# Kernel optimization log

Hardware: AMD Instinct MI355X
Metric: run time of the kernel (lower is better)

## Reference

```python
import jax, jax.numpy as jnp
import numpy as np

B, T, IN, Z, S = 256, 1024, 64, 512, 2
H = Z - S  # 510
MHU = 1.5


def setup_inputs() -> dict:
    key = jax.random.key(0)
    ks = jax.random.split(key, 12)
    sc = 0.05
    return {
        "rnn_input": jax.random.normal(ks[0], (B, T, IN), jnp.float32),
        "tau": jax.random.uniform(ks[1], (B, T, 1), jnp.float32),
        "z0": jax.random.normal(ks[2], (1, B, Z), jnp.float32),
        "cz0": jax.random.normal(ks[3], (1, B, Z), jnp.float32),
        # LSTMCell: W: (IN+S) -> 4H with bias, U: H -> 4H no bias
        "W_w": jax.random.normal(ks[4], (4 * H, IN + S), jnp.float32) * sc,
        "W_b": jax.random.normal(ks[5], (4 * H,), jnp.float32) * sc,
        "U_w": jax.random.normal(ks[6], (4 * H, H), jnp.float32) * sc,
        "alpha_w": jax.random.normal(ks[7], (S, H), jnp.float32) * sc,
        "alpha_b": jax.random.normal(ks[8], (S,), jnp.float32) * sc,
        "hx_w": jax.random.normal(ks[9], (S, H), jnp.float32) * sc,
        "hx_b": jax.random.normal(ks[10], (S,), jnp.float32) * sc,
    }


def reference(rnn_input, tau, z0, cz0, W_w, W_b, U_w, alpha_w, alpha_b, hx_w, hx_b):
    dt = rnn_input.dtype
    # fixed continuous-time system matrix (state_dim = 2)
    A = jnp.array([[MHU, -MHU], [1.0 / MHU, 0.0]], dtype=dt)

    x0 = z0[0, :, :S]       # [B, S]
    h0 = z0[0, :, S:]       # [B, H]
    c0 = cz0[0, :, S:]      # [B, H]
    cx = cz0[0, :, :S]      # [B, S], carried unchanged

    def step(carry, xs):
        x_prev, h, c = carry
        inp_t, tau_t = xs                                   # [B,IN], [B,1]
        u = jnp.concatenate([x_prev, inp_t], axis=1)        # [B, S+IN]
        gates = u @ W_w.T + W_b + h @ U_w.T                 # [B, 4H]
        i, f, g, o = jnp.split(gates, 4, axis=1)
        i = jax.nn.sigmoid(i)
        f = jax.nn.sigmoid(f)
        g = jnp.tanh(g)
        o = jax.nn.sigmoid(o)
        c_new = f * c + i * g
        h_new = o * jnp.tanh(c_new)
        # forward-Euler discretisation: x_mid = (I + tau*A) x_prev
        x_mid = x_prev + tau_t * (x_prev @ A.T)             # [B, S]
        alpha = jax.nn.sigmoid(h_new @ alpha_w.T + alpha_b) # [B, S]
        x_next = (1.0 - alpha) * x_mid + alpha * (h_new @ hx_w.T + hx_b)
        out = jnp.concatenate([x_next, h_new], axis=1)      # [B, Z]
        return (x_next, h_new, c_new), out

    xs = (jnp.swapaxes(rnn_input, 0, 1), jnp.swapaxes(tau, 0, 1))  # time-major
    (xT, hT, cT), outs = jax.lax.scan(step, (x0, h0, c0), xs)
    outputs = jnp.swapaxes(outs, 0, 1)                      # [B, T, Z]
    z_fin = jnp.concatenate([xT, hT], axis=1)[None]         # [1, B, Z]
    cz_fin = jnp.concatenate([cx, cT], axis=1)[None]        # [1, B, Z]
    return outputs, (z_fin, cz_fin)
```

## Files before the change

kernel.cpp:

```cpp
#include <hip/hip_runtime.h>

typedef unsigned short u16;
typedef unsigned int u32;
typedef unsigned long long u64;
typedef __attribute__((ext_vector_type(8))) short s16x8;
typedef __attribute__((ext_vector_type(4))) short s16x4;
typedef __attribute__((ext_vector_type(4))) float f32x4;

#define TSTEPS 1024
#define PSTR   584
#define ZOFF   ((size_t)134217728)
#define CZOFF  (ZOFF + 131072)

#define CNT_OFF 0
#define HB_OFF  1024
#define WK_OFF  525312
#define WX_OFF  2884608
#define WB_OFF  2900992
#define AW_OFF  2909184
#define AB_OFF  2913280

__device__ __forceinline__ float bf2f(u16 h) { union { unsigned u; float f; } c; c.u = ((unsigned)h) << 16; return c.f; }
__device__ __forceinline__ u16 f2bf(float f) { union { float f; unsigned u; } c; c.f = f; unsigned u = c.u; return (u16)((u + 0x7FFFu + ((u >> 16) & 1u)) >> 16); }
__device__ __forceinline__ float fsigm(float x) { return __builtin_amdgcn_rcpf(1.f + __builtin_amdgcn_exp2f(-1.44269504089f * x)); }
__device__ __forceinline__ float ftanh(float x) { float t = __builtin_amdgcn_exp2f(2.88539008178f * x); return 1.f - 2.f * __builtin_amdgcn_rcpf(t + 1.f); }
__device__ __forceinline__ float pick4(float a, float b, float c, float d, int m) {
  return (m == 0) ? a : (m == 1) ? b : (m == 2) ? c : d;
}
#define NTS(p, v) __builtin_nontemporal_store((v), (p))

#if defined(__has_builtin)
#if __has_builtin(__builtin_amdgcn_fdot2_f32_bf16)
#define HAVE_DOT2 1
typedef __bf16 bf16x2 __attribute__((ext_vector_type(2)));
#endif
#endif

__device__ __forceinline__ float dot2acc(u32 h2, u32 a2, float acc) {
#ifdef HAVE_DOT2
  bf16x2 hv, av;
  __builtin_memcpy(&hv, &h2, 4);
  __builtin_memcpy(&av, &a2, 4);
  return __builtin_amdgcn_fdot2_f32_bf16(hv, av, acc, false);
#else
  acc += bf2f((u16)(h2 & 0xFFFFu)) * bf2f((u16)(a2 & 0xFFFFu));
  acc += bf2f((u16)(h2 >> 16)) * bf2f((u16)(a2 >> 16));
  return acc;
#endif
}

__global__ void prep_pack(const float* __restrict__ W_w, const float* __restrict__ W_b,
                          const float* __restrict__ U_w, const float* __restrict__ alpha_w,
                          const float* __restrict__ alpha_b, const float* __restrict__ hx_w,
                          const float* __restrict__ hx_b,
                          u16* __restrict__ wk, float* __restrict__ wx, float* __restrict__ wb,
                          u16* __restrict__ aw, float* __restrict__ ab, unsigned* __restrict__ cnt)
{
  int n = blockIdx.x;
  int tid = threadIdx.x;
  if (n < 2048) {
    int j = n >> 2, g = n & 3;
    bool real = (j < 510);
    int row = g * 510 + j;
    for (int k = tid; k < 576; k += 64) {
      float v = 0.f;
      if (real) {
        if (k < 64) v = W_w[row * 66 + 2 + k];
        else { int kk = k - 64; v = (kk < 510) ? U_w[row * 510 + kk] : 0.f; }
      }
      wk[(size_t)n * 576 + k] = f2bf(v);
    }
    if (tid == 0) {
      wx[n * 2 + 0] = real ? W_w[row * 66 + 0] : 0.f;
      wx[n * 2 + 1] = real ? W_w[row * 66 + 1] : 0.f;
      wb[n] = real ? W_b[row] : 0.f;
    }
    if (n == 0 && tid < 16)
      __hip_atomic_store(&cnt[tid * 16], 0u, __ATOMIC_RELAXED, __HIP_MEMORY_SCOPE_AGENT);
  } else {
    int s = n - 2048;
    for (int j = tid; j < 512; j += 64) {
      float v = 0.f;
      if (j < 510) v = (s < 2) ? alpha_w[s * 510 + j] : hx_w[(s - 2) * 510 + j];
      aw[s * 512 + j] = f2bf(v);
    }
    if (tid == 0) ab[s] = (s < 2) ? alpha_b[s] : hx_b[s - 2];
  }
}

__global__ void prep_h0(const float* __restrict__ z0, u16* __restrict__ hb0)
{
  int b = blockIdx.x;
  int j = threadIdx.x * 4;
#pragma unroll
  for (int e = 0; e < 4; ++e) {
    int jj = j + e;
    hb0[(size_t)b * 512 + jj] = (jj < 510) ? f2bf(z0[(size_t)b * 512 + 2 + jj]) : (u16)0;
  }
}

extern "C" __global__ void __launch_bounds__(256, 1)
lstm_persist(const float* __restrict__ rnn, const float* __restrict__ tau,
             const float* __restrict__ z0, const float* __restrict__ cz0,
             const u16* __restrict__ wk, const float* __restrict__ wx, const float* __restrict__ wb,
             const u16* __restrict__ aw, const float* __restrict__ ab,
             u16* __restrict__ hbuf, unsigned* __restrict__ cnt,
             float* __restrict__ out)
{
  __shared__ u16   u_sh[16 * PSTR];
  __shared__ float xs_sh[16 * 2];

  const int tid = threadIdx.x;
  const int bid = blockIdx.x;
  const int grp = bid & 15;
  const int w   = bid >> 4;
  const int bb0 = grp * 16;
  const int v   = tid >> 6;
  const int l   = tid & 63;
  const int l15 = l & 15, l4 = l >> 4;
  const int n0  = w * 128 + v * 32;
  const int prow = tid >> 4;
  const int jc   = tid & 15;

  u32 awr[4][4][4];
  {
    const u32* awp = (const u32*)aw;
#pragma unroll
    for (int s = 0; s < 4; ++s)
#pragma unroll
      for (int q = 0; q < 4; ++q)
#pragma unroll
        for (int p = 0; p < 4; ++p)
          awr[s][q][p] = awp[(s * 512 + jc * 32 + q * 8) / 2 + p];
  }
  float ab0 = ab[0], ab1 = ab[1], ab2 = ab[2], ab3 = ab[3];

  s16x8 bfr[36];
  {
    const u16* wb0 = wk + (size_t)(n0 + l15) * 576 + l4 * 8;
#pragma unroll
    for (int kf = 0; kf < 18; ++kf) {
      bfr[2 * kf + 0] = *(const s16x8*)(wb0 + kf * 32);
      bfr[2 * kf + 1] = *(const s16x8*)(wb0 + 16 * 576 + kf * 32);
    }
  }
  float wxf[2][2], wbf[2];
  {
    int nA = n0 + l15, nB = nA + 16;
    wxf[0][0] = wx[nA * 2]; wxf[0][1] = wx[nA * 2 + 1];
    wxf[1][0] = wx[nB * 2]; wxf[1][1] = wx[nB * 2 + 1];
    wbf[0] = wb[nA]; wbf[1] = wb[nB];
  }
  float cst[2][4];
#pragma unroll
  for (int nf = 0; nf < 2; ++nf) {
    int j = (n0 + nf * 16 + l15) >> 2;
#pragma unroll
    for (int r = 0; r < 4; ++r) {
      int b = bb0 + 4 * l4 + r;
      cst[nf][r] = (j < 510) ? cz0[(size_t)b * 512 + 2 + j] : 0.f;
    }
  }
  {
    const float* ip = rnn + (size_t)(bb0 + prow) * (TSTEPS * 64) + jc * 4;
    float4 inpv = *(const float4*)ip;
    s16x4 iv;
    iv[0] = (short)f2bf(inpv.x); iv[1] = (short)f2bf(inpv.y);
    iv[2] = (short)f2bf(inpv.z); iv[3] = (short)f2bf(inpv.w);
    *(s16x4*)(&u_sh[prow * PSTR + jc * 4]) = iv;
  }
  __syncthreads();

  const int g = l & 3;
  const float sc_a = (g == 2) ? -2.88539008178f : -1.44269504089f;
  const float sc_m = (g == 2) ? 2.f : 1.f;
  const float sc_c = (g == 2) ? -1.f : 0.f;

  unsigned* mycnt = cnt + grp * 16;
  float tv_reg = 0.f;

  for (int t = 0; t <= TSTEPS; ++t) {
    u16* hb = hbuf + (size_t)(t & 1) * (256 * 512) + (size_t)bb0 * 512;
    u64 q0, q1, q2, q3, q4, q5, q6, q7;
    {
      u64* hp = (u64*)hb + (size_t)tid * 8;
      q0 = __hip_atomic_load(hp + 0, __ATOMIC_RELAXED, __HIP_MEMORY_SCOPE_AGENT);
      q1 = __hip_atomic_load(hp + 1, __ATOMIC_RELAXED, __HIP_MEMORY_SCOPE_AGENT);
      q2 = __hip_atomic_load(hp + 2, __ATOMIC_RELAXED, __HIP_MEMORY_SCOPE_AGENT);
      q3 = __hip_atomic_load(hp + 3, __ATOMIC_RELAXED, __HIP_MEMORY_SCOPE_AGENT);
      q4 = __hip_atomic_load(hp + 4, __ATOMIC_RELAXED, __HIP_MEMORY_SCOPE_AGENT);
      q5 = __hip_atomic_load(hp + 5, __ATOMIC_RELAXED, __HIP_MEMORY_SCOPE_AGENT);
      q6 = __hip_atomic_load(hp + 6, __ATOMIC_RELAXED, __HIP_MEMORY_SCOPE_AGENT);
      q7 = __hip_atomic_load(hp + 7, __ATOMIC_RELAXED, __HIP_MEMORY_SCOPE_AGENT);
    }
    u32 h32[16];
    h32[0] = (u32)q0; h32[1] = (u32)(q0 >> 32); h32[2]  = (u32)q1; h32[3]  = (u32)(q1 >> 32);
    h32[4] = (u32)q2; h32[5] = (u32)(q2 >> 32); h32[6]  = (u32)q3; h32[7]  = (u32)(q3 >> 32);
    h32[8] = (u32)q4; h32[9] = (u32)(q4 >> 32); h32[10] = (u32)q5; h32[11] = (u32)(q5 >> 32);
    h32[12] = (u32)q6; h32[13] = (u32)(q6 >> 32); h32[14] = (u32)q7; h32[15] = (u32)(q7 >> 32);

    float s0 = 0.f, s1 = 0.f, s2 = 0.f, s3 = 0.f;
#pragma unroll
    for (int q = 0; q < 4; ++q) {
#pragma unroll
      for (int p = 0; p < 4; ++p) {
        u32 h2 = h32[4 * q + p];
        s0 = dot2acc(h2, awr[0][q][p], s0);
        s1 = dot2acc(h2, awr[1][q][p], s1);
        s2 = dot2acc(h2, awr[2][q][p], s2);
        s3 = dot2acc(h2, awr[3][q][p], s3);
      }
    }
#pragma unroll
    for (int m = 1; m <= 8; m <<= 1) {
      s0 += __shfl_xor(s0, m, 64);
      s1 += __shfl_xor(s1, m, 64);
      s2 += __shfl_xor(s2, m, 64);
      s3 += __shfl_xor(s3, m, 64);
    }
    {
      u16* ur = &u_sh[prow * PSTR + 64 + jc * 32];
      u64 t2[2];
      t2[0] = q0; t2[1] = q1; __builtin_memcpy(ur + 0, t2, 16);
      t2[0] = q2; t2[1] = q3; __builtin_memcpy(ur + 8, t2, 16);
      t2[0] = q4; t2[1] = q5; __builtin_memcpy(ur + 16, t2, 16);
      t2[0] = q6; t2[1] = q7; __builtin_memcpy(ur + 24, t2, 16);
    }
    if ((l & 15) == 0) {
      int row = prow;
      float xn0, xn1;
      if (t == 0) {
        xn0 = z0[(size_t)(bb0 + row) * 512 + 0];
        xn1 = z0[(size_t)(bb0 + row) * 512 + 1];
      } else {
        float x0p = xs_sh[row * 2 + 0], x1p = xs_sh[row * 2 + 1];
        float tv = tv_reg;
        float a0v = fsigm(s0 + ab0);
        float a1v = fsigm(s1 + ab1);
        float hx0 = s2 + ab2, hx1 = s3 + ab3;
        float xm0 = x0p + tv * (1.5f * x0p - 1.5f * x1p);
        float xm1 = x1p + tv * (0.6666666667f * x0p);
        xn0 = (1.f - a0v) * xm0 + a0v * hx0;
        xn1 = (1.f - a1v) * xm1 + a1v * hx1;
      }
      xs_sh[row * 2 + 0] = xn0; xs_sh[row * 2 + 1] = xn1;
    }
    __syncthreads();

    if (t == TSTEPS) {
      int j2 = tid * 2;
      if (j2 < 510) {
        unsigned hv2 = *(const unsigned*)&u_sh[w * PSTR + 64 + j2];
        float h0 = bf2f((u16)(hv2 & 0xFFFFu));
        float h1 = bf2f((u16)(hv2 >> 16));
        size_t ob = ((size_t)(bb0 + w) * TSTEPS + (TSTEPS - 1)) * 512 + 2 + j2;
        NTS(&out[ob], h0); NTS(&out[ob + 1], h1);
        size_t zb = ZOFF + (size_t)(bb0 + w) * 512 + 2 + j2;
        NTS(&out[zb], h0); NTS(&out[zb + 1], h1);
      }
      if ((l & 15) == 0 && w == prow) {
        int b = bb0 + prow;
        float xn0 = xs_sh[prow * 2 + 0], xn1 = xs_sh[prow * 2 + 1];
        float* ob = out + ((size_t)b * TSTEPS + (TSTEPS - 1)) * 512;
        NTS(ob + 0, xn0); NTS(ob + 1, xn1);
        NTS(&out[ZOFF + (size_t)b * 512 + 0], xn0);
        NTS(&out[ZOFF + (size_t)b * 512 + 1], xn1);
        NTS(&out[CZOFF + (size_t)b * 512 + 0], cz0[(size_t)b * 512 + 0]);
        NTS(&out[CZOFF + (size_t)b * 512 + 1], cz0[(size_t)b * 512 + 1]);
      }
      break;
    }

    f32x4 acc0 = {0.f, 0.f, 0.f, 0.f};
    f32x4 acc1 = {0.f, 0.f, 0.f, 0.f};
    {
      const u16* ap = &u_sh[l15 * PSTR + l4 * 8];
#pragma unroll
      for (int kf = 0; kf < 18; ++kf) {
        s16x8 a = *(const s16x8*)(ap + kf * 32);
        acc0 = __builtin_amdgcn_mfma_f32_16x16x32_bf16(a, bfr[2 * kf + 0], acc0, 0, 0, 0);
        acc1 = __builtin_amdgcn_mfma_f32_16x16x32_bf16(a, bfr[2 * kf + 1], acc1, 0, 0, 0);
      }
    }
    u16* hout = hbuf + (size_t)((t + 1) & 1) * (256 * 512);
    float xr[4][2];
#pragma unroll
    for (int r = 0; r < 4; ++r) {
      xr[r][0] = xs_sh[(4 * l4 + r) * 2 + 0];
      xr[r][1] = xs_sh[(4 * l4 + r) * 2 + 1];
    }
    float myh0 = 0.f, myh1 = 0.f;
#pragma unroll
    for (int nf = 0; nf < 2; ++nf) {
      f32x4 av = nf ? acc1 : acc0;
#pragma unroll
      for (int r = 0; r < 4; ++r) {
        float pre = av[r] + wbf[nf] + xr[r][0] * wxf[nf][0] + xr[r][1] * wxf[nf][1];
        float y = __builtin_amdgcn_rcpf(1.f + __builtin_amdgcn_exp2f(sc_a * pre));
        float act = y * sc_m + sc_c;
        float vB = __shfl_xor(act, 1, 64);
        float vC = __shfl_xor(act, 2, 64);
        float vD = __shfl_xor(vB, 2, 64);
        float si = pick4(act, vB, vC, vD, g);
        float sf = pick4(act, vB, vC, vD, g ^ 1);
        float tg = pick4(act, vB, vC, vD, g ^ 2);
        float so = pick4(act, vB, vC, vD, g ^ 3);
        float cn = sf * cst[nf][r] + si * tg;
        cst[nf][r] = cn;
        float hn = so * ftanh(cn);
        if (g == r) { if (nf == 0) myh0 = hn; else myh1 = hn; }
      }
    }
    {
      int row = 4 * l4 + g;
      u32 mine = (u32)f2bf(myh0) | ((u32)f2bf(myh1) << 16);
      u32 oth = (u32)__shfl_xor((int)mine, 4, 64);
      if (((l15 >> 2) & 1) == 0) {
        int j0 = (n0 >> 2) + (l15 >> 2);
        u32 v0 = (mine & 0xFFFFu) | ((oth & 0xFFFFu) << 16);
        u32 v1 = (mine >> 16) | (oth & 0xFFFF0000u);
        u32* hp = (u32*)(hout + (size_t)(bb0 + row) * 512);
        __hip_atomic_store(hp + (j0 >> 1), v0, __ATOMIC_RELAXED, __HIP_MEMORY_SCOPE_AGENT);
        __hip_atomic_store(hp + (j0 >> 1) + 2, v1, __ATOMIC_RELAXED, __HIP_MEMORY_SCOPE_AGENT);
      }
    }
    __syncthreads();
    if (tid == 0) {
      asm volatile("s_waitcnt vmcnt(0)" ::: "memory");
      __hip_atomic_fetch_add(mycnt, 1u, __ATOMIC_RELAXED, __HIP_MEMORY_SCOPE_AGENT);
    }
    if (t >= 1) {
      int j2 = tid * 2;
      if (j2 < 510) {
        unsigned hv2 = *(const unsigned*)&u_sh[w * PSTR + 64 + j2];
        float h0 = bf2f((u16)(hv2 & 0xFFFFu));
        float h1 = bf2f((u16)(hv2 >> 16));
        size_t ob = ((size_t)(bb0 + w) * TSTEPS + (t - 1)) * 512 + 2 + j2;
        NTS(&out[ob], h0); NTS(&out[ob + 1], h1);
      }
      if ((l & 15) == 0 && w == prow) {
        float* ob = out + ((size_t)(bb0 + prow) * TSTEPS + (t - 1)) * 512;
        NTS(ob + 0, xs_sh[prow * 2 + 0]); NTS(ob + 1, xs_sh[prow * 2 + 1]);
      }
    }
    if (t + 1 < TSTEPS) {
      const float* ip = rnn + (size_t)(bb0 + prow) * (TSTEPS * 64) + (size_t)(t + 1) * 64 + jc * 4;
      float4 inpv = *(const float4*)ip;
      s16x4 iv;
      iv[0] = (short)f2bf(inpv.x); iv[1] = (short)f2bf(inpv.y);
      iv[2] = (short)f2bf(inpv.z); iv[3] = (short)f2bf(inpv.w);
      *(s16x4*)(&u_sh[prow * PSTR + jc * 4]) = iv;
    }
    if ((l & 15) == 0) {
      tv_reg = tau[(size_t)(bb0 + prow) * TSTEPS + t];
    }
    if (tid == 0) {
      unsigned tgt = 16u * (unsigned)(t + 1);
      while (__hip_atomic_load(mycnt, __ATOMIC_RELAXED, __HIP_MEMORY_SCOPE_AGENT) < tgt) {
        __builtin_amdgcn_s_sleep(1);
      }
    }
    __syncthreads();
  }

#pragma unroll
  for (int nf = 0; nf < 2; ++nf) {
    int j = (n0 + nf * 16 + l15) >> 2;
    if (j < 510) {
#pragma unroll
      for (int r = 0; r < 4; ++r) {
        if ((l & 3) == r) {
          NTS(&out[CZOFF + (size_t)(bb0 + 4 * l4 + r) * 512 + 2 + j], cst[nf][r]);
        }
      }
    }
  }
}

extern "C" void kernel_launch(void* const* d_in, const int* in_sizes, int n_in,
                              void* d_out, int out_size, void* d_ws, size_t ws_size,
                              hipStream_t stream) {
  const float* rnn     = (const float*)d_in[0];
  const float* tau     = (const float*)d_in[1];
  const float* z0      = (const float*)d_in[2];
  const float* cz0     = (const float*)d_in[3];
  const float* W_w     = (const float*)d_in[4];
  const float* W_b     = (const float*)d_in[5];
  const float* U_w     = (const float*)d_in[6];
  const float* alpha_w = (const float*)d_in[7];
  const float* alpha_b = (const float*)d_in[8];
  const float* hx_w    = (const float*)d_in[9];
  const float* hx_b    = (const float*)d_in[10];

  char* ws = (char*)d_ws;
  unsigned* cnt = (unsigned*)(ws + CNT_OFF);
  u16*      hb  = (u16*)(ws + HB_OFF);
  u16*      wk  = (u16*)(ws + WK_OFF);
  float*    wx  = (float*)(ws + WX_OFF);
  float*    wbv = (float*)(ws + WB_OFF);
  u16*      awv = (u16*)(ws + AW_OFF);
  float*    abv = (float*)(ws + AB_OFF);

  hipLaunchKernelGGL(prep_pack, dim3(2052), dim3(64), 0, stream,
                     W_w, W_b, U_w, alpha_w, alpha_b, hx_w, hx_b, wk, wx, wbv, awv, abv, cnt);
  hipLaunchKernelGGL(prep_h0, dim3(256), dim3(128), 0, stream, z0, hb);
  hipLaunchKernelGGL(lstm_persist, dim3(256), dim3(256), 0, stream,
                     rnn, tau, z0, cz0, wk, wx, wbv, awv, abv, hb, cnt, (float*)d_out);
}
```

Baseline: 5.441 ms.

## Replace block-wide barrier spin with per-wave counters and double-buffered shared state

```diff
diff --git a/kernel.cpp b/kernel.cpp
--- a/kernel.cpp
+++ b/kernel.cpp
@@ -13,12 +13,12 @@
 #define CZOFF  (ZOFF + 131072)
 
 #define CNT_OFF 0
-#define HB_OFF  1024
-#define WK_OFF  525312
-#define WX_OFF  2884608
-#define WB_OFF  2900992
-#define AW_OFF  2909184
-#define AB_OFF  2913280
+#define HB_OFF  4096
+#define WK_OFF  (HB_OFF + 524288)
+#define WX_OFF  (WK_OFF + 2359296)
+#define WB_OFF  (WX_OFF + 16384)
+#define AW_OFF  (WB_OFF + 8192)
+#define AB_OFF  (AW_OFF + 4096)
 
 __device__ __forceinline__ float bf2f(u16 h) { union { unsigned u; float f; } c; c.u = ((unsigned)h) << 16; return c.f; }
 __device__ __forceinline__ u16 f2bf(float f) { union { float f; unsigned u; } c; c.f = f; unsigned u = c.u; return (u16)((u + 0x7FFFu + ((u >> 16) & 1u)) >> 16); }
@@ -28,6 +28,7 @@
   return (m == 0) ? a : (m == 1) ? b : (m == 2) ? c : d;
 }
 #define NTS(p, v) __builtin_nontemporal_store((v), (p))
+#define AL(p) __hip_atomic_load((p), __ATOMIC_RELAXED, __HIP_MEMORY_SCOPE_AGENT)
 
 #if defined(__has_builtin)
 #if __has_builtin(__builtin_amdgcn_fdot2_f32_bf16)
@@ -75,7 +76,7 @@
       wx[n * 2 + 1] = real ? W_w[row * 66 + 1] : 0.f;
       wb[n] = real ? W_b[row] : 0.f;
     }
-    if (n == 0 && tid < 16)
+    if (n == 0)
       __hip_atomic_store(&cnt[tid * 16], 0u, __ATOMIC_RELAXED, __HIP_MEMORY_SCOPE_AGENT);
   } else {
     int s = n - 2048;
@@ -107,8 +108,8 @@
              u16* __restrict__ hbuf, unsigned* __restrict__ cnt,
              float* __restrict__ out)
 {
-  __shared__ u16   u_sh[16 * PSTR];
-  __shared__ float xs_sh[16 * 2];
+  __shared__ u16   u_sh[2][16 * PSTR];
+  __shared__ float xs_sh[2][16 * 2];
 
   const int tid = threadIdx.x;
   const int bid = blockIdx.x;
@@ -167,7 +168,7 @@
     s16x4 iv;
     iv[0] = (short)f2bf(inpv.x); iv[1] = (short)f2bf(inpv.y);
     iv[2] = (short)f2bf(inpv.z); iv[3] = (short)f2bf(inpv.w);
-    *(s16x4*)(&u_sh[prow * PSTR + jc * 4]) = iv;
+    *(s16x4*)(&u_sh[0][prow * PSTR + jc * 4]) = iv;
   }
   __syncthreads();
 
@@ -176,22 +177,29 @@
   const float sc_m = (g == 2) ? 2.f : 1.f;
   const float sc_c = (g == 2) ? -1.f : 0.f;
 
-  unsigned* mycnt = cnt + grp * 16;
+  unsigned* cvec = cnt + grp * 64;
+  unsigned* myslot = cvec + v * 16;
   float tv_reg = 0.f;
 
   for (int t = 0; t <= TSTEPS; ++t) {
-    u16* hb = hbuf + (size_t)(t & 1) * (256 * 512) + (size_t)bb0 * 512;
+    const int cur = t & 1;
+    if (t > 0) {
+      unsigned tgt = 16u * (unsigned)t;
+      for (;;) {
+        u32 c0 = AL(cvec + 0);
+        u32 c1 = AL(cvec + 16);
+        u32 c2 = AL(cvec + 32);
+        u32 c3 = AL(cvec + 48);
+        if ((c0 >= tgt) & (c1 >= tgt) & (c2 >= tgt) & (c3 >= tgt)) break;
+      }
+      asm volatile("" ::: "memory");
+    }
+    u16* hb = hbuf + (size_t)cur * (256 * 512) + (size_t)bb0 * 512;
     u64 q0, q1, q2, q3, q4, q5, q6, q7;
     {
       u64* hp = (u64*)hb + (size_t)tid * 8;
-      q0 = __hip_atomic_load(hp + 0, __ATOMIC_RELAXED, __HIP_MEMORY_SCOPE_AGENT);
-      q1 = __hip_atomic_load(hp + 1, __ATOMIC_RELAXED, __HIP_MEMORY_SCOPE_AGENT);
-      q2 = __hip_atomic_load(hp + 2, __ATOMIC_RELAXED, __HIP_MEMORY_SCOPE_AGENT);
-      q3 = __hip_atomic_load(hp + 3, __ATOMIC_RELAXED, __HIP_MEMORY_SCOPE_AGENT);
-      q4 = __hip_atomic_load(hp + 4, __ATOMIC_RELAXED, __HIP_MEMORY_SCOPE_AGENT);
-      q5 = __hip_atomic_load(hp + 5, __ATOMIC_RELAXED, __HIP_MEMORY_SCOPE_AGENT);
-      q6 = __hip_atomic_load(hp + 6, __ATOMIC_RELAXED, __HIP_MEMORY_SCOPE_AGENT);
-      q7 = __hip_atomic_load(hp + 7, __ATOMIC_RELAXED, __HIP_MEMORY_SCOPE_AGENT);
+      q0 = AL(hp + 0); q1 = AL(hp + 1); q2 = AL(hp + 2); q3 = AL(hp + 3);
+      q4 = AL(hp + 4); q5 = AL(hp + 5); q6 = AL(hp + 6); q7 = AL(hp + 7);
     }
     u32 h32[16];
     h32[0] = (u32)q0; h32[1] = (u32)(q0 >> 32); h32[2]  = (u32)q1; h32[3]  = (u32)(q1 >> 32);
@@ -219,7 +227,7 @@
       s3 += __shfl_xor(s3, m, 64);
     }
     {
-      u16* ur = &u_sh[prow * PSTR + 64 + jc * 32];
+      u16* ur = &u_sh[cur][prow * PSTR + 64 + jc * 32];
       u64 t2[2];
       t2[0] = q0; t2[1] = q1; __builtin_memcpy(ur + 0, t2, 16);
       t2[0] = q2; t2[1] = q3; __builtin_memcpy(ur + 8, t2, 16);
@@ -233,7 +241,7 @@
         xn0 = z0[(size_t)(bb0 + row) * 512 + 0];
         xn1 = z0[(size_t)(bb0 + row) * 512 + 1];
       } else {
-        float x0p = xs_sh[row * 2 + 0], x1p = xs_sh[row * 2 + 1];
+        float x0p = xs_sh[cur ^ 1][row * 2 + 0], x1p = xs_sh[cur ^ 1][row * 2 + 1];
         float tv = tv_reg;
         float a0v = fsigm(s0 + ab0);
         float a1v = fsigm(s1 + ab1);
@@ -243,14 +251,14 @@
         xn0 = (1.f - a0v) * xm0 + a0v * hx0;
         xn1 = (1.f - a1v) * xm1 + a1v * hx1;
       }
-      xs_sh[row * 2 + 0] = xn0; xs_sh[row * 2 + 1] = xn1;
+      xs_sh[cur][row * 2 + 0] = xn0; xs_sh[cur][row * 2 + 1] = xn1;
     }
     __syncthreads();
 
     if (t == TSTEPS) {
       int j2 = tid * 2;
       if (j2 < 510) {
-        unsigned hv2 = *(const unsigned*)&u_sh[w * PSTR + 64 + j2];
+        unsigned hv2 = *(const unsigned*)&u_sh[cur][w * PSTR + 64 + j2];
         float h0 = bf2f((u16)(hv2 & 0xFFFFu));
         float h1 = bf2f((u16)(hv2 >> 16));
         size_t ob = ((size_t)(bb0 + w) * TSTEPS + (TSTEPS - 1)) * 512 + 2 + j2;
@@ -260,7 +268,7 @@
       }
       if ((l & 15) == 0 && w == prow) {
         int b = bb0 + prow;
-        float xn0 = xs_sh[prow * 2 + 0], xn1 = xs_sh[prow * 2 + 1];
+        float xn0 = xs_sh[cur][prow * 2 + 0], xn1 = xs_sh[cur][prow * 2 + 1];
         float* ob = out + ((size_t)b * TSTEPS + (TSTEPS - 1)) * 512;
         NTS(ob + 0, xn0); NTS(ob + 1, xn1);
         NTS(&out[ZOFF + (size_t)b * 512 + 0], xn0);
@@ -274,7 +282,7 @@
     f32x4 acc0 = {0.f, 0.f, 0.f, 0.f};
     f32x4 acc1 = {0.f, 0.f, 0.f, 0.f};
     {
-      const u16* ap = &u_sh[l15 * PSTR + l4 * 8];
+      const u16* ap = &u_sh[cur][l15 * PSTR + l4 * 8];
 #pragma unroll
       for (int kf = 0; kf < 18; ++kf) {
         s16x8 a = *(const s16x8*)(ap + kf * 32);
@@ -282,12 +290,12 @@
         acc1 = __builtin_amdgcn_mfma_f32_16x16x32_bf16(a, bfr[2 * kf + 1], acc1, 0, 0, 0);
       }
     }
-    u16* hout = hbuf + (size_t)((t + 1) & 1) * (256 * 512);
+    u16* hout = hbuf + (size_t)(cur ^ 1) * (256 * 512);
     float xr[4][2];
 #pragma unroll
     for (int r = 0; r < 4; ++r) {
-      xr[r][0] = xs_sh[(4 * l4 + r) * 2 + 0];
-      xr[r][1] = xs_sh[(4 * l4 + r) * 2 + 1];
+      xr[r][0] = xs_sh[cur][(4 * l4 + r) * 2 + 0];
+      xr[r][1] = xs_sh[cur][(4 * l4 + r) * 2 + 1];
     }
     float myh0 = 0.f, myh1 = 0.f;
 #pragma unroll
@@ -324,15 +332,13 @@
         __hip_atomic_store(hp + (j0 >> 1) + 2, v1, __ATOMIC_RELAXED, __HIP_MEMORY_SCOPE_AGENT);
       }
     }
-    __syncthreads();
-    if (tid == 0) {
-      asm volatile("s_waitcnt vmcnt(0)" ::: "memory");
-      __hip_atomic_fetch_add(mycnt, 1u, __ATOMIC_RELAXED, __HIP_MEMORY_SCOPE_AGENT);
-    }
+    asm volatile("s_waitcnt vmcnt(0)" ::: "memory");
+    if (l == 0)
+      __hip_atomic_fetch_add(myslot, 1u, __ATOMIC_RELAXED, __HIP_MEMORY_SCOPE_AGENT);
     if (t >= 1) {
       int j2 = tid * 2;
       if (j2 < 510) {
-        unsigned hv2 = *(const unsigned*)&u_sh[w * PSTR + 64 + j2];
+        unsigned hv2 = *(const unsigned*)&u_sh[cur][w * PSTR + 64 + j2];
         float h0 = bf2f((u16)(hv2 & 0xFFFFu));
         float h1 = bf2f((u16)(hv2 >> 16));
         size_t ob = ((size_t)(bb0 + w) * TSTEPS + (t - 1)) * 512 + 2 + j2;
@@ -340,7 +346,7 @@
       }
       if ((l & 15) == 0 && w == prow) {
         float* ob = out + ((size_t)(bb0 + prow) * TSTEPS + (t - 1)) * 512;
-        NTS(ob + 0, xs_sh[prow * 2 + 0]); NTS(ob + 1, xs_sh[prow * 2 + 1]);
+        NTS(ob + 0, xs_sh[cur][prow * 2 + 0]); NTS(ob + 1, xs_sh[cur][prow * 2 + 1]);
       }
     }
     if (t + 1 < TSTEPS) {
@@ -349,18 +355,11 @@
       s16x4 iv;
       iv[0] = (short)f2bf(inpv.x); iv[1] = (short)f2bf(inpv.y);
       iv[2] = (short)f2bf(inpv.z); iv[3] = (short)f2bf(inpv.w);
-      *(s16x4*)(&u_sh[prow * PSTR + jc * 4]) = iv;
+      *(s16x4*)(&u_sh[cur ^ 1][prow * PSTR + jc * 4]) = iv;
     }
     if ((l & 15) == 0) {
       tv_reg = tau[(size_t)(bb0 + prow) * TSTEPS + t];
     }
-    if (tid == 0) {
-      unsigned tgt = 16u * (unsigned)(t + 1);
-      while (__hip_atomic_load(mycnt, __ATOMIC_RELAXED, __HIP_MEMORY_SCOPE_AGENT) < tgt) {
-        __builtin_amdgcn_s_sleep(1);
-      }
-    }
-    __syncthreads();
   }
 
 #pragma unroll
```

After: 5.492 ms. Within noise of the previous version (+0.9%).

## Replace atomic counter barrier with per-block step flags polled at step start

Applied to the files above, without the earlier changes.

```diff
diff --git a/kernel.cpp b/kernel.cpp
--- a/kernel.cpp
+++ b/kernel.cpp
@@ -6,13 +6,14 @@
 typedef __attribute__((ext_vector_type(8))) short s16x8;
 typedef __attribute__((ext_vector_type(4))) short s16x4;
 typedef __attribute__((ext_vector_type(4))) float f32x4;
+typedef __attribute__((ext_vector_type(2))) float f32x2;
 
 #define TSTEPS 1024
 #define PSTR   584
 #define ZOFF   ((size_t)134217728)
 #define CZOFF  (ZOFF + 131072)
 
-#define CNT_OFF 0
+#define ST_OFF  0
 #define HB_OFF  1024
 #define WK_OFF  525312
 #define WX_OFF  2884608
@@ -54,7 +55,7 @@
                           const float* __restrict__ alpha_b, const float* __restrict__ hx_w,
                           const float* __restrict__ hx_b,
                           u16* __restrict__ wk, float* __restrict__ wx, float* __restrict__ wb,
-                          u16* __restrict__ aw, float* __restrict__ ab, unsigned* __restrict__ cnt)
+                          u16* __restrict__ aw, float* __restrict__ ab, u32* __restrict__ stmp)
 {
   int n = blockIdx.x;
   int tid = threadIdx.x;
@@ -75,8 +76,11 @@
       wx[n * 2 + 1] = real ? W_w[row * 66 + 1] : 0.f;
       wb[n] = real ? W_b[row] : 0.f;
     }
-    if (n == 0 && tid < 16)
-      __hip_atomic_store(&cnt[tid * 16], 0u, __ATOMIC_RELAXED, __HIP_MEMORY_SCOPE_AGENT);
+    if (n == 0) {
+#pragma unroll
+      for (int k = 0; k < 4; ++k)
+        __hip_atomic_store(&stmp[tid * 4 + k], 0u, __ATOMIC_RELAXED, __HIP_MEMORY_SCOPE_AGENT);
+    }
   } else {
     int s = n - 2048;
     for (int j = tid; j < 512; j += 64) {
@@ -104,11 +108,11 @@
              const float* __restrict__ z0, const float* __restrict__ cz0,
              const u16* __restrict__ wk, const float* __restrict__ wx, const float* __restrict__ wb,
              const u16* __restrict__ aw, const float* __restrict__ ab,
-             u16* __restrict__ hbuf, unsigned* __restrict__ cnt,
+             u16* __restrict__ hbuf, u32* __restrict__ stmp,
              float* __restrict__ out)
 {
   __shared__ u16   u_sh[16 * PSTR];
-  __shared__ float xs_sh[16 * 2];
+  __shared__ float xs_sh[2][32];
 
   const int tid = threadIdx.x;
   const int bid = blockIdx.x;
@@ -176,11 +180,20 @@
   const float sc_m = (g == 2) ? 2.f : 1.f;
   const float sc_c = (g == 2) ? -1.f : 0.f;
 
-  unsigned* mycnt = cnt + grp * 16;
+  u32* sl = stmp + grp * 16;
   float tv_reg = 0.f;
 
   for (int t = 0; t <= TSTEPS; ++t) {
-    u16* hb = hbuf + (size_t)(t & 1) * (256 * 512) + (size_t)bb0 * 512;
+    const int cur = t & 1;
+    if (t > 0) {
+      const u32 tgt = (u32)t;
+      for (;;) {
+        u32 sv = __hip_atomic_load(&sl[jc], __ATOMIC_RELAXED, __HIP_MEMORY_SCOPE_AGENT);
+        if (__ballot(sv >= tgt) == ~0ull) break;
+      }
+      asm volatile("" ::: "memory");
+    }
+    u16* hb = hbuf + (size_t)cur * (256 * 512) + (size_t)bb0 * 512;
     u64 q0, q1, q2, q3, q4, q5, q6, q7;
     {
       u64* hp = (u64*)hb + (size_t)tid * 8;
@@ -199,6 +212,21 @@
     h32[8] = (u32)q4; h32[9] = (u32)(q4 >> 32); h32[10] = (u32)q5; h32[11] = (u32)(q5 >> 32);
     h32[12] = (u32)q6; h32[13] = (u32)(q6 >> 32); h32[14] = (u32)q7; h32[15] = (u32)(q7 >> 32);
 
+    if (t >= 1 && prow == w) {
+      float* ob = out + ((size_t)(bb0 + w) * TSTEPS + (t - 1)) * 512 + 2 + jc * 32;
+#pragma unroll
+      for (int p = 0; p < 16; ++p) {
+        int col = jc * 32 + 2 * p;
+        if (col < 510) {
+          u32 h2 = h32[p];
+          f32x2 fv;
+          fv[0] = bf2f((u16)(h2 & 0xFFFFu));
+          fv[1] = bf2f((u16)(h2 >> 16));
+          NTS((f32x2*)(ob + 2 * p), fv);
+        }
+      }
+    }
+
     float s0 = 0.f, s1 = 0.f, s2 = 0.f, s3 = 0.f;
 #pragma unroll
     for (int q = 0; q < 4; ++q) {
@@ -233,7 +261,7 @@
         xn0 = z0[(size_t)(bb0 + row) * 512 + 0];
         xn1 = z0[(size_t)(bb0 + row) * 512 + 1];
       } else {
-        float x0p = xs_sh[row * 2 + 0], x1p = xs_sh[row * 2 + 1];
+        float x0p = xs_sh[cur ^ 1][row * 2 + 0], x1p = xs_sh[cur ^ 1][row * 2 + 1];
         float tv = tv_reg;
         float a0v = fsigm(s0 + ab0);
         float a1v = fsigm(s1 + ab1);
@@ -243,7 +271,7 @@
         xn0 = (1.f - a0v) * xm0 + a0v * hx0;
         xn1 = (1.f - a1v) * xm1 + a1v * hx1;
       }
-      xs_sh[row * 2 + 0] = xn0; xs_sh[row * 2 + 1] = xn1;
+      xs_sh[cur][row * 2 + 0] = xn0; xs_sh[cur][row * 2 + 1] = xn1;
     }
     __syncthreads();
 
@@ -253,14 +281,12 @@
         unsigned hv2 = *(const unsigned*)&u_sh[w * PSTR + 64 + j2];
         float h0 = bf2f((u16)(hv2 & 0xFFFFu));
         float h1 = bf2f((u16)(hv2 >> 16));
-        size_t ob = ((size_t)(bb0 + w) * TSTEPS + (TSTEPS - 1)) * 512 + 2 + j2;
-        NTS(&out[ob], h0); NTS(&out[ob + 1], h1);
         size_t zb = ZOFF + (size_t)(bb0 + w) * 512 + 2 + j2;
         NTS(&out[zb], h0); NTS(&out[zb + 1], h1);
       }
       if ((l & 15) == 0 && w == prow) {
         int b = bb0 + prow;
-        float xn0 = xs_sh[prow * 2 + 0], xn1 = xs_sh[prow * 2 + 1];
+        float xn0 = xs_sh[cur][prow * 2 + 0], xn1 = xs_sh[cur][prow * 2 + 1];
         float* ob = out + ((size_t)b * TSTEPS + (TSTEPS - 1)) * 512;
         NTS(ob + 0, xn0); NTS(ob + 1, xn1);
         NTS(&out[ZOFF + (size_t)b * 512 + 0], xn0);
@@ -282,12 +308,12 @@
         acc1 = __builtin_amdgcn_mfma_f32_16x16x32_bf16(a, bfr[2 * kf + 1], acc1, 0, 0, 0);
       }
     }
-    u16* hout = hbuf + (size_t)((t + 1) & 1) * (256 * 512);
+    u16* hout = hbuf + (size_t)(cur ^ 1) * (256 * 512);
     float xr[4][2];
 #pragma unroll
     for (int r = 0; r < 4; ++r) {
-      xr[r][0] = xs_sh[(4 * l4 + r) * 2 + 0];
-      xr[r][1] = xs_sh[(4 * l4 + r) * 2 + 1];
+      xr[r][0] = xs_sh[cur][(4 * l4 + r) * 2 + 0];
+      xr[r][1] = xs_sh[cur][(4 * l4 + r) * 2 + 1];
     }
     float myh0 = 0.f, myh1 = 0.f;
 #pragma unroll
@@ -327,21 +353,11 @@
     __syncthreads();
     if (tid == 0) {
       asm volatile("s_waitcnt vmcnt(0)" ::: "memory");
-      __hip_atomic_fetch_add(mycnt, 1u, __ATOMIC_RELAXED, __HIP_MEMORY_SCOPE_AGENT);
-    }
-    if (t >= 1) {
-      int j2 = tid * 2;
-      if (j2 < 510) {
-        unsigned hv2 = *(const unsigned*)&u_sh[w * PSTR + 64 + j2];
-        float h0 = bf2f((u16)(hv2 & 0xFFFFu));
-        float h1 = bf2f((u16)(hv2 >> 16));
-        size_t ob = ((size_t)(bb0 + w) * TSTEPS + (t - 1)) * 512 + 2 + j2;
-        NTS(&out[ob], h0); NTS(&out[ob + 1], h1);
-      }
-      if ((l & 15) == 0 && w == prow) {
-        float* ob = out + ((size_t)(bb0 + prow) * TSTEPS + (t - 1)) * 512;
-        NTS(ob + 0, xs_sh[prow * 2 + 0]); NTS(ob + 1, xs_sh[prow * 2 + 1]);
-      }
+      __hip_atomic_store(&sl[w], (u32)(t + 1), __ATOMIC_RELAXED, __HIP_MEMORY_SCOPE_AGENT);
+    }
+    if (t >= 1 && (l & 15) == 0 && w == prow) {
+      float* ob = out + ((size_t)(bb0 + prow) * TSTEPS + (t - 1)) * 512;
+      NTS(ob + 0, xs_sh[cur][prow * 2 + 0]); NTS(ob + 1, xs_sh[cur][prow * 2 + 1]);
     }
     if (t + 1 < TSTEPS) {
       const float* ip = rnn + (size_t)(bb0 + prow) * (TSTEPS * 64) + (size_t)(t + 1) * 64 + jc * 4;
@@ -354,13 +370,6 @@
     if ((l & 15) == 0) {
       tv_reg = tau[(size_t)(bb0 + prow) * TSTEPS + t];
     }
-    if (tid == 0) {
-      unsigned tgt = 16u * (unsigned)(t + 1);
-      while (__hip_atomic_load(mycnt, __ATOMIC_RELAXED, __HIP_MEMORY_SCOPE_AGENT) < tgt) {
-        __builtin_amdgcn_s_sleep(1);
-      }
-    }
-    __syncthreads();
   }
 
 #pragma unroll
@@ -393,17 +402,17 @@
   const float* hx_b    = (const float*)d_in[10];
 
   char* ws = (char*)d_ws;
-  unsigned* cnt = (unsigned*)(ws + CNT_OFF);
+  u32*      st  = (u32*)(ws + ST_OFF);
   u16*      hb  = (u16*)(ws + HB_OFF);
-  u16*      wk  = (u16*)(ws + WK_OFF);
-  float*    wx  = (float*)(ws + WX_OFF);
+  u16*      wkv = (u16*)(ws + WK_OFF);
+  float*    wxv = (float*)(ws + WX_OFF);
   float*    wbv = (float*)(ws + WB_OFF);
   u16*      awv = (u16*)(ws + AW_OFF);
   float*    abv = (float*)(ws + AB_OFF);
 
   hipLaunchKernelGGL(prep_pack, dim3(2052), dim3(64), 0, stream,
-                     W_w, W_b, U_w, alpha_w, alpha_b, hx_w, hx_b, wk, wx, wbv, awv, abv, cnt);
+                     W_w, W_b, U_w, alpha_w, alpha_b, hx_w, hx_b, wkv, wxv, wbv, awv, abv, st);
   hipLaunchKernelGGL(prep_h0, dim3(256), dim3(128), 0, stream, z0, hb);
   hipLaunchKernelGGL(lstm_persist, dim3(256), dim3(256), 0, stream,
-                     rnn, tau, z0, cz0, wk, wx, wbv, awv, abv, hb, cnt, (float*)d_out);
-}
+                     rnn, tau, z0, cz0, wkv, wxv, wbv, awv, abv, hb, st, (float*)d_out);
+}
```

Result: slower. 5.922 ms (+8.9%).
